# Kernel tuning notes

Measured on AMD Instinct MI355X. Metric: run time of the kernel, lower is better.

## Reference

```python
import jax, jax.numpy as jnp
import numpy as np

EMBED = 512
HEADS = 8
EPS = 1e-5


def setup_inputs() -> dict:
    key = jax.random.key(0)
    ks = jax.random.split(key, 8)
    B, Sq, Skv, D = 4, 2048, 2048, EMBED
    return {
        "layer_input": jax.random.normal(ks[0], (B, Sq, D), jnp.float32),
        "cross_attn_input": jax.random.normal(ks[1], (B, Skv, D), jnp.float32),
        "Wq": jax.random.normal(ks[2], (D, D), jnp.float32) * (D ** -0.5),
        "bq": jnp.zeros((D,), jnp.float32),
        "Wkv": jax.random.normal(ks[3], (D, 2 * D), jnp.float32) * (D ** -0.5),
        "bkv": jnp.zeros((2 * D,), jnp.float32),
        "Wo": jax.random.normal(ks[4], (D, D), jnp.float32) * (D ** -0.5),
        "bo": jnp.zeros((D,), jnp.float32),
        "gamma": jnp.ones((D,), jnp.float32),
        "beta": jnp.zeros((D,), jnp.float32),
    }


def _split_heads(x):
    # ... s (h d) -> ... h s d
    *lead, s, hd = x.shape
    d = hd // HEADS
    return jnp.moveaxis(x.reshape(*lead, s, HEADS, d), -2, -3)


def _merge_heads(x):
    # ... h s d -> ... s (h d)
    x = jnp.moveaxis(x, -3, -2)
    *lead, s, h, d = x.shape
    return x.reshape(*lead, s, h * d)


def reference(layer_input, cross_attn_input, Wq, bq, Wkv, bkv, Wo, bo, gamma, beta):
    scale = (EMBED // HEADS) ** -0.5
    res = layer_input
    q = layer_input @ Wq + bq
    kv = cross_attn_input @ Wkv + bkv
    k, v = jnp.split(kv, 2, axis=-1)
    q, k, v = map(_split_heads, (q, k, v))  # [B, H, S, d]
    scores = jnp.einsum('bhqc,bhkc->bhqk', q, k) * scale
    weights = jax.nn.softmax(scores, axis=-1)  # dropout p=0 -> identity
    out = jnp.einsum('bhqk,bhkc->bhqc', weights, v)
    out = _merge_heads(out)
    out = out @ Wo + bo
    x = out + res
    mu = jnp.mean(x, axis=-1, keepdims=True)
    var = jnp.mean(jnp.square(x - mu), axis=-1, keepdims=True)
    return (x - mu) * jax.lax.rsqrt(var + EPS) * gamma + beta
```

## Files before the change

kernel.cpp:

```cpp
#include <hip/hip_runtime.h>
#include <hip/hip_bf16.h>
#include <stdint.h>

#define SEQ    2048
#define DM     512
#define NHEAD  8
#define HD     64
#define BATCH  4
#define MTOT   (BATCH*SEQ)

typedef __attribute__((ext_vector_type(4))) float  f32x4;
typedef __attribute__((ext_vector_type(8))) short  bf16x8;
typedef __attribute__((ext_vector_type(8))) unsigned short u16x8;
typedef __attribute__((ext_vector_type(4))) unsigned short u16x4;
typedef __attribute__((ext_vector_type(4))) float  fl4;
typedef __attribute__((ext_vector_type(2))) unsigned u32x2;
typedef __attribute__((ext_vector_type(4))) unsigned u32x4;

__device__ __forceinline__ unsigned short f2bf(float f) {
  union { float f; unsigned u; } c; c.f = f;
  return (unsigned short)((c.u + 0x7fffu + ((c.u >> 16) & 1u)) >> 16);
}

__device__ __forceinline__ void load_lds16(const void* g, void* l) {
  __builtin_amdgcn_global_load_lds((__attribute__((address_space(1))) void*)g,
                                   (__attribute__((address_space(3))) void*)l,
                                   16, 0, 0);
}

__device__ __forceinline__ u32x2 ds_tr16(const void* p) {
  u32x2 r;
  asm volatile("ds_read_b64_tr_b16 %0, %1"
               : "=v"(r)
               : "v"((__attribute__((address_space(3))) const void*)p));
  return r;
}

__device__ __forceinline__ unsigned pack_bf2(float lo, float hi) {
  __hip_bfloat162 h2 = __float22bfloat162_rn(float2{lo, hi});
  unsigned u; __builtin_memcpy(&u, &h2, 4);
  return u;
}

__global__ void k_pre(const float* __restrict__ X, unsigned short* __restrict__ Xb,
                      const float* __restrict__ C, unsigned short* __restrict__ Cb,
                      const float* __restrict__ Wq, unsigned short* __restrict__ Wqt,
                      const float* __restrict__ Wkv, unsigned short* __restrict__ Wkvt,
                      const float* __restrict__ Wo, unsigned short* __restrict__ Wot) {
  __shared__ __align__(16) unsigned short t[64][66];
  int bid = blockIdx.x, tid = threadIdx.x;
  if (bid < 8192) {
    const float* src = (bid < 4096) ? X : C;
    unsigned short* dst = (bid < 4096) ? Xb : Cb;
    int i = (bid & 4095) * 256 + tid;
    fl4 v = *(const fl4*)(src + (size_t)i * 4);
    u32x2 o;
    o[0] = pack_bf2(v[0], v[1]);
    o[1] = pack_bf2(v[2], v[3]);
    *(u32x2*)((void*)(dst + (size_t)i * 4)) = o;
    return;
  }
  int tjob = bid - 8192;
  const float* W; unsigned short* Wt; int Nd, bx, by;
  if (tjob < 64)       { W = Wq;  Wt = Wqt;  Nd = 512;  bx = tjob & 7;  by = tjob >> 3; }
  else if (tjob < 192) { int u = tjob - 64;  W = Wkv; Wt = Wkvt; Nd = 1024; bx = u & 15; by = u >> 4; }
  else                 { int u = tjob - 192; W = Wo;  Wt = Wot;  Nd = 512;  bx = u & 7;  by = u >> 3; }
  int k0 = by * 64, n0 = bx * 64;
  int r = tid >> 2, cs = (tid & 3) * 16;
  const float* src = W + (size_t)(k0 + r) * Nd + n0 + cs;
#pragma unroll
  for (int i = 0; i < 4; ++i) {
    fl4 v = *(const fl4*)(src + i * 4);
    *(unsigned*)&t[r][cs + i*4]     = pack_bf2(v[0], v[1]);
    *(unsigned*)&t[r][cs + i*4 + 2] = pack_bf2(v[2], v[3]);
  }
  __syncthreads();
  unsigned short* drow = Wt + (size_t)(n0 + r) * 512 + k0 + cs;
#pragma unroll
  for (int half = 0; half < 2; ++half) {
    u16x8 o;
#pragma unroll
    for (int i = 0; i < 8; ++i) o[i] = t[cs + half*8 + i][r];
    *(u16x8*)(drow + half * 8) = o;
  }
}

template<int RESID>
__device__ __forceinline__ void gemm128x64(
    const unsigned short* __restrict__ A,
    const unsigned short* __restrict__ Bt,
    const float* __restrict__ bias,
    const float* __restrict__ res,
    void* __restrict__ Cout,
    int N, int K, int m0, int n0, float osc,
    unsigned short* Als, unsigned short* Bls) {
  int tid  = threadIdx.x;
  int lane = tid & 63, wave = tid >> 6;
  int q = lane & 15, lk = lane >> 4;
  f32x4 acc[2][4];
#pragma unroll
  for (int mt = 0; mt < 2; ++mt)
#pragma unroll
    for (int nt = 0; nt < 4; ++nt) acc[mt][nt] = f32x4{0.f,0.f,0.f,0.f};

  const unsigned short* gA[4];
#pragma unroll
  for (int it = 0; it < 4; ++it) {
    int idx = tid + it * 256;
    int row = idx >> 3, ch = idx & 7, sc = ch ^ (row & 7);
    gA[it] = A + (size_t)(m0 + row) * K + sc * 8;
  }
  const unsigned short* gB[2];
#pragma unroll
  for (int it = 0; it < 2; ++it) {
    int idx = tid + it * 256;
    int row = idx >> 3, ch = idx & 7, sc = ch ^ (row & 7);
    gB[it] = Bt + (size_t)(n0 + row) * K + sc * 8;
  }
  char* aD = (char*)Als + tid * 16;
  char* bD = (char*)Bls + tid * 16;

#pragma unroll
  for (int it = 0; it < 4; ++it) { load_lds16(gA[it], aD + it * 4096); gA[it] += 64; }
#pragma unroll
  for (int it = 0; it < 2; ++it) { load_lds16(gB[it], bD + it * 4096); gB[it] += 64; }
  __syncthreads();

  int nkb = K >> 6;
  int buf = 0;
  for (int kb = 0; kb < nkb; ++kb) {
    if (kb + 1 < nkb) {
      char* aN = aD + (buf ^ 1) * 16384;
      char* bN = bD + (buf ^ 1) * 8192;
#pragma unroll
      for (int it = 0; it < 4; ++it) { load_lds16(gA[it], aN + it * 4096); gA[it] += 64; }
#pragma unroll
      for (int it = 0; it < 2; ++it) { load_lds16(gB[it], bN + it * 4096); gB[it] += 64; }
    }
    const char* aR = (const char*)Als + buf * 16384;
    const char* bR = (const char*)Bls + buf * 8192;
#pragma unroll
    for (int ks = 0; ks < 2; ++ks) {
      bf16x8 a[2], b[4];
#pragma unroll
      for (int mt = 0; mt < 2; ++mt) {
        int row = wave * 32 + mt * 16 + q;
        a[mt] = *(const bf16x8*)(aR + row * 128 + (((ks*4 + lk) ^ (row & 7)) * 16));
      }
#pragma unroll
      for (int nt = 0; nt < 4; ++nt) {
        int row = nt * 16 + q;
        b[nt] = *(const bf16x8*)(bR + row * 128 + (((ks*4 + lk) ^ (row & 7)) * 16));
      }
#pragma unroll
      for (int mt = 0; mt < 2; ++mt)
#pragma unroll
        for (int nt = 0; nt < 4; ++nt)
          acc[mt][nt] = __builtin_amdgcn_mfma_f32_16x16x32_bf16(a[mt], b[nt], acc[mt][nt], 0, 0, 0);
    }
    __syncthreads();
    buf ^= 1;
  }
#pragma unroll
  for (int nt = 0; nt < 4; ++nt) {
    int col = n0 + nt * 16 + q;
    float bv = bias[col];
#pragma unroll
    for (int mt = 0; mt < 2; ++mt) {
      int rowb = m0 + wave * 32 + mt * 16 + lk * 4;
#pragma unroll
      for (int rr = 0; rr < 4; ++rr) {
        float v = acc[mt][nt][rr] + bv;
        size_t off = (size_t)(rowb + rr) * N + col;
        if (RESID) ((float*)Cout)[off] = v + res[off];
        else       ((unsigned short*)Cout)[off] = f2bf(v * osc);
      }
    }
  }
}

__global__ __launch_bounds__(256, 3)
void k_projmm(const unsigned short* __restrict__ Xb, const unsigned short* __restrict__ Cb,
              const unsigned short* __restrict__ Wqt, const unsigned short* __restrict__ Wkvt,
              const float* __restrict__ bq, const float* __restrict__ bkv,
              unsigned short* __restrict__ Qb, unsigned short* __restrict__ KVb) {
  __shared__ __align__(16) unsigned short Als[2 * 128 * 64];
  __shared__ __align__(16) unsigned short Bls[2 * 64 * 64];
  int bid = blockIdx.x;
  int l = (bid & 7) * 192 + (bid >> 3);
  const float c1 = 0.125f * 1.44269504088896340736f;
  if (l < 512) {
    int m = l >> 3, n = l & 7;
    gemm128x64<0>(Xb, Wqt, bq, nullptr, Qb, 512, 512, m * 128, n * 64, c1, Als, Bls);
  } else {
    int l2 = l - 512;
    int m = l2 >> 4, n = l2 & 15;
    gemm128x64<0>(Cb, Wkvt, bkv, nullptr, KVb, 1024, 512, m * 128, n * 64, 1.0f, Als, Bls);
  }
}

__global__ __launch_bounds__(256, 3)
void k_omm(const unsigned short* __restrict__ Abuf, const unsigned short* __restrict__ Wot,
           const float* __restrict__ bo, const float* __restrict__ resid,
           float* __restrict__ tmp) {
  __shared__ __align__(16) unsigned short Als[2 * 128 * 64];
  __shared__ __align__(16) unsigned short Bls[2 * 64 * 64];
  int bid = blockIdx.x;
  int l = (bid & 7) * 64 + (bid >> 3);
  int m = l >> 3, n = l & 7;
  gemm128x64<1>(Abuf, Wot, bo, resid, tmp, 512, 512, m * 128, n * 64, 1.0f, Als, Bls);
}

__global__ __launch_bounds__(256, 4)
void k_attn(const unsigned short* __restrict__ Qb,
            const unsigned short* __restrict__ KVb,
            unsigned short* __restrict__ Ab) {
  __shared__ __align__(16) unsigned short Klds[2][64 * 64];
  __shared__ __align__(16) unsigned short Vlds[3][4096];
  int tid  = threadIdx.x;
  int lane = tid & 63, wave = tid >> 6;
  int q    = lane & 15, lk = lane >> 4;
  int lkb0 = lk & 1, lkb1 = lk >> 1;
  int bid = blockIdx.x;
  int swz = (bid & 7) * 128 + (bid >> 3);
  int qt = swz & 31, bh = swz >> 5;
  int b  = bh >> 3, h = bh & 7;
  int q0 = qt * 64 + wave * 16;
  const size_t kvbase = (size_t)b * SEQ * 1024;

  bf16x8 qf0, qf1;
  {
    size_t qrow = (size_t)b * SEQ + q0 + q;
    qf0 = *(const bf16x8*)(Qb + qrow * DM + h * HD + lk * 8);
    qf1 = *(const bf16x8*)(Qb + qrow * DM + h * HD + 32 + lk * 8);
  }
  f32x4 acc[4];
#pragma unroll
  for (int i = 0; i < 4; ++i) acc[i] = f32x4{0.f,0.f,0.f,0.f};
  float l = 0.f;
  u32x4 pbA[2];

  const unsigned short *gK0, *gK1, *gV0, *gV1;
  {
    int r0 = tid >> 3, s0_ = (tid & 7) ^ (r0 & 7);
    gK0 = KVb + kvbase + (size_t)r0 * 1024 + h * HD + s0_ * 8;
    int i1 = tid + 256, r1 = i1 >> 3, s1_ = (i1 & 7) ^ (r1 & 7);
    gK1 = KVb + kvbase + (size_t)r1 * 1024 + h * HD + s1_ * 8;
    int dt0 = tid >> 7, w0 = tid & 127, p0 = w0 >> 1, c80 = (w0 & 1) * 8;
    int t0 = (p0 & 32) + (((p0 >> 2) & 3) << 3) + (((p0 >> 4) & 1) << 2) + (p0 & 3);
    gV0 = KVb + kvbase + (size_t)t0 * 1024 + 512 + h * HD + dt0 * 16 + c80;
    int i1v = tid + 256, dt1 = i1v >> 7, w1 = i1v & 127, p1 = w1 >> 1, c81 = (w1 & 1) * 8;
    int t1 = (p1 & 32) + (((p1 >> 2) & 3) << 3) + (((p1 >> 4) & 1) << 2) + (p1 & 3);
    gV1 = KVb + kvbase + (size_t)t1 * 1024 + 512 + h * HD + dt1 * 16 + c81;
  }
  char* kdA = (char*)Klds[0] + tid * 16;
  char* kdB = (char*)Klds[1] + tid * 16;
  char* vdA = (char*)Vlds[0] + tid * 16;
  char* vdB = (char*)Vlds[1] + tid * 16;
  char* vdC = (char*)Vlds[2] + tid * 16;
  const char* krA = (const char*)Klds[0];
  const char* krB = (const char*)Klds[1];
  const char* vsA = (const char*)Vlds[0] + lane * 8;
  const char* vsB = (const char*)Vlds[1] + lane * 8;
  const char* vsC = (const char*)Vlds[2] + lane * 8;

#define STAGE(kd_, vd_) do {                        \
    load_lds16(gK0, (kd_));                         \
    load_lds16(gK1, (kd_) + 4096);                  \
    load_lds16(gV0, (vd_));                         \
    load_lds16(gV1, (vd_) + 4096);                  \
    gK0 += 65536; gK1 += 65536;                     \
    gV0 += 65536; gV1 += 65536;                     \
  } while (0)

  STAGE(kdA, vdA);
  __syncthreads();

  const int NT = SEQ / 64;
  int kc = 0;
  int vn = 1;
  int vp = 2;
  for (int kb = 0; kb < NT; ++kb) {
    if (kb < NT - 1) {
      char* kd = kc ? kdA : kdB;
      char* vd = (vn == 0) ? vdA : ((vn == 1) ? vdB : vdC);
      STAGE(kd, vd);
    }

    u32x2 tr[4][2][2];
    if (kb > 0) {
      const char* vsrc = (vp == 0) ? vsA : ((vp == 1) ? vsB : vsC);
#pragma unroll
      for (int dt = 0; dt < 4; ++dt)
#pragma unroll
        for (int ks2 = 0; ks2 < 2; ++ks2)
#pragma unroll
          for (int u = 0; u < 2; ++u)
            tr[dt][ks2][u] = ds_tr16(vsrc + dt * 2048 + ks2 * 1024 + u * 512);
      asm volatile("s_waitcnt lgkmcnt(0)" ::: "memory");
      __builtin_amdgcn_sched_barrier(0);
      __builtin_amdgcn_s_setprio(1);
#pragma unroll
      for (int ks2 = 0; ks2 < 2; ++ks2) {
        union { u32x4 u; bf16x8 v; } pb;
        pb.u = pbA[ks2];
#pragma unroll
        for (int dt = 0; dt < 4; ++dt) {
          union { u32x4 u; bf16x8 v; } cv;
          cv.u[0] = tr[dt][ks2][0][0]; cv.u[1] = tr[dt][ks2][0][1];
          cv.u[2] = tr[dt][ks2][1][0]; cv.u[3] = tr[dt][ks2][1][1];
          acc[dt] = __builtin_amdgcn_mfma_f32_16x16x32_bf16(cv.v, pb.v, acc[dt], 0, 0, 0);
        }
      }
      __builtin_amdgcn_s_setprio(0);
    }

    const char* kr = kc ? krB : krA;
    f32x4 st[4];
#pragma unroll
    for (int kt = 0; kt < 4; ++kt) st[kt] = f32x4{0.f,0.f,0.f,0.f};
    __builtin_amdgcn_s_setprio(1);
#pragma unroll
    for (int kt = 0; kt < 4; ++kt) {
      int row = kt * 16 + q;
      bf16x8 kf0 = *(const bf16x8*)(kr + row * 128 + ((lk ^ (row & 7)) * 16));
      bf16x8 kf1 = *(const bf16x8*)(kr + row * 128 + (((4 + lk) ^ (row & 7)) * 16));
      st[kt] = __builtin_amdgcn_mfma_f32_16x16x32_bf16(kf0, qf0, st[kt], 0, 0, 0);
      st[kt] = __builtin_amdgcn_mfma_f32_16x16x32_bf16(kf1, qf1, st[kt], 0, 0, 0);
    }
    __builtin_amdgcn_s_setprio(0);

    float p[4][4];
#pragma unroll
    for (int kt = 0; kt < 4; ++kt)
#pragma unroll
      for (int r = 0; r < 4; ++r) {
        float pe = __builtin_amdgcn_exp2f(st[kt][r]);
        p[kt][r] = pe;
        l += pe;
      }
    unsigned pk[4][2];
#pragma unroll
    for (int kt = 0; kt < 4; ++kt)
#pragma unroll
      for (int rr = 0; rr < 2; ++rr)
        pk[kt][rr] = pack_bf2(p[kt][2*rr], p[kt][2*rr + 1]);
#pragma unroll
    for (int ks2 = 0; ks2 < 2; ++ks2)
#pragma unroll
      for (int rr = 0; rr < 2; ++rr) {
        unsigned a_ = pk[2*ks2][rr], b_ = pk[2*ks2 + 1][rr];
        unsigned E = lkb1 ? b_ : a_;
        unsigned O = lkb1 ? a_ : b_;
        unsigned A = __shfl_xor((int)E, 16);
        unsigned B = __shfl_xor((int)O, 32);
        unsigned C = __shfl_xor((int)O, 48);
        unsigned dlo = lkb1 ? (lkb0 ? A : B) : (lkb0 ? C : E);
        unsigned dhi = lkb1 ? (lkb0 ? E : C) : (lkb0 ? B : A);
        pbA[ks2][rr]     = dlo;
        pbA[ks2][2 + rr] = dhi;
      }

    __syncthreads();
    kc ^= 1;
    vn = (vn == 2) ? 0 : vn + 1;
    vp = (vp == 2) ? 0 : vp + 1;
  }

  {
    const char* vsrc = (vp == 0) ? vsA : ((vp == 1) ? vsB : vsC);
    u32x2 tr[4][2][2];
#pragma unroll
    for (int dt = 0; dt < 4; ++dt)
#pragma unroll
      for (int ks2 = 0; ks2 < 2; ++ks2)
#pragma unroll
        for (int u = 0; u < 2; ++u)
          tr[dt][ks2][u] = ds_tr16(vsrc + dt * 2048 + ks2 * 1024 + u * 512);
    asm volatile("s_waitcnt lgkmcnt(0)" ::: "memory");
    __builtin_amdgcn_sched_barrier(0);
#pragma unroll
    for (int ks2 = 0; ks2 < 2; ++ks2) {
      union { u32x4 u; bf16x8 v; } pb;
      pb.u = pbA[ks2];
#pragma unroll
      for (int dt = 0; dt < 4; ++dt) {
        union { u32x4 u; bf16x8 v; } cv;
        cv.u[0] = tr[dt][ks2][0][0]; cv.u[1] = tr[dt][ks2][0][1];
        cv.u[2] = tr[dt][ks2][1][0]; cv.u[3] = tr[dt][ks2][1][1];
        acc[dt] = __builtin_amdgcn_mfma_f32_16x16x32_bf16(cv.v, pb.v, acc[dt], 0, 0, 0);
      }
    }
  }

  l += __shfl_xor(l, 16);
  l += __shfl_xor(l, 32);

  float inv = 1.0f / l;
  size_t orow = ((size_t)b * SEQ + q0 + q) * DM + h * HD + lk * 4;
#pragma unroll
  for (int dt = 0; dt < 4; ++dt) {
    u16x4 o;
#pragma unroll
    for (int r = 0; r < 4; ++r) o[r] = f2bf(acc[dt][r] * inv);
    *(u16x4*)(Ab + orow + dt * 16) = o;
  }
#undef STAGE
}

__global__ void k_ln(const float* __restrict__ x, const float* __restrict__ gamma,
                     const float* __restrict__ beta, float* __restrict__ out) {
  int tid = threadIdx.x, lane = tid & 63, wave = tid >> 6;
  size_t row = (size_t)blockIdx.x * 4 + wave;
  const float* xr = x + row * DM + lane * 8;
  fl4 v0 = *(const fl4*)xr;
  fl4 v1 = *(const fl4*)(xr + 4);
  float s  = (v0[0]+v0[1]) + (v0[2]+v0[3]) + (v1[0]+v1[1]) + (v1[2]+v1[3]);
  float ss = (v0[0]*v0[0]+v0[1]*v0[1]) + (v0[2]*v0[2]+v0[3]*v0[3])
           + (v1[0]*v1[0]+v1[1]*v1[1]) + (v1[2]*v1[2]+v1[3]*v1[3]);
#pragma unroll
  for (int off = 1; off < 64; off <<= 1) {
    s  += __shfl_xor(s, off);
    ss += __shfl_xor(ss, off);
  }
  float mu  = s * (1.0f / DM);
  float var = ss * (1.0f / DM) - mu * mu;
  float w = rsqrtf(var + 1e-5f);
  fl4 g0 = *(const fl4*)(gamma + lane*8), g1 = *(const fl4*)(gamma + lane*8 + 4);
  fl4 b0 = *(const fl4*)(beta + lane*8),  b1 = *(const fl4*)(beta + lane*8 + 4);
  fl4 o0, o1;
#pragma unroll
  for (int i = 0; i < 4; ++i) {
    o0[i] = (v0[i] - mu) * w * g0[i] + b0[i];
    o1[i] = (v1[i] - mu) * w * g1[i] + b1[i];
  }
  float* orow = out + row * DM + lane * 8;
  *(fl4*)orow = o0;
  *(fl4*)(orow + 4) = o1;
}

extern "C" void kernel_launch(void* const* d_in, const int* in_sizes, int n_in,
                              void* d_out, int out_size, void* d_ws, size_t ws_size,
                              hipStream_t stream) {
  const float* layer_input = (const float*)d_in[0];
  const float* cross       = (const float*)d_in[1];
  const float* Wq   = (const float*)d_in[2];
  const float* bq   = (const float*)d_in[3];
  const float* Wkv  = (const float*)d_in[4];
  const float* bkv  = (const float*)d_in[5];
  const float* Wo   = (const float*)d_in[6];
  const float* bo   = (const float*)d_in[7];
  const float* gamma = (const float*)d_in[8];
  const float* beta  = (const float*)d_in[9];
  float* out = (float*)d_out;

  char* ws = (char*)d_ws;
  unsigned short* Xb   = (unsigned short*)(ws + (size_t)0);
  unsigned short* Cb   = (unsigned short*)(ws + ((size_t)8  << 20));
  unsigned short* Qb   = (unsigned short*)(ws + ((size_t)16 << 20));
  unsigned short* KVb  = (unsigned short*)(ws + ((size_t)24 << 20));
  unsigned short* Abuf = (unsigned short*)(ws + ((size_t)40 << 20));
  float*          tmp  = (float*)         (ws + ((size_t)48 << 20));
  unsigned short* Wqt  = (unsigned short*)(ws + ((size_t)64 << 20));
  unsigned short* Wkvt = (unsigned short*)(ws + ((size_t)65 << 20));
  unsigned short* Wot  = (unsigned short*)(ws + ((size_t)67 << 20));

  k_pre<<<8448, 256, 0, stream>>>(layer_input, Xb, cross, Cb,
                                  Wq, Wqt, Wkv, Wkvt, Wo, Wot);
  k_projmm<<<1536, 256, 0, stream>>>(Xb, Cb, Wqt, Wkvt, bq, bkv, Qb, KVb);
  k_attn<<<1024, 256, 0, stream>>>(Qb, KVb, Abuf);
  k_omm<<<512, 256, 0, stream>>>(Abuf, Wot, bo, layer_input, tmp);
  k_ln<<<MTOT/4, 256, 0, stream>>>(tmp, gamma, beta, out);
}
```

Measured before the change: 116.1 us.

## Process two 16-row query subtiles per wave in attention kernel

Each wave now handles 32 query rows (two 16-row halves) instead of 16, so every block covers a 128-query tile and the grid halves to 512 blocks. K and V fragments loaded from LDS are reused across both query halves, which halves the K/V global and LDS traffic per query row. The cost is roughly double the accumulator and score registers, so launch bounds drop to 2 blocks per CU. With only 512 blocks there is less parallelism to hide latency.

```diff
diff --git a/kernel.cpp b/kernel.cpp
--- a/kernel.cpp
+++ b/kernel.cpp
@@ -211,7 +211,7 @@
   gemm128x64<1>(Abuf, Wot, bo, resid, tmp, 512, 512, m * 128, n * 64, 1.0f, Als, Bls);
 }
 
-__global__ __launch_bounds__(256, 4)
+__global__ __launch_bounds__(256, 2)
 void k_attn(const unsigned short* __restrict__ Qb,
             const unsigned short* __restrict__ KVb,
             unsigned short* __restrict__ Ab) {
@@ -222,23 +222,26 @@
   int q    = lane & 15, lk = lane >> 4;
   int lkb0 = lk & 1, lkb1 = lk >> 1;
   int bid = blockIdx.x;
-  int swz = (bid & 7) * 128 + (bid >> 3);
-  int qt = swz & 31, bh = swz >> 5;
+  int swz = (bid & 7) * 64 + (bid >> 3);
+  int qt = swz & 15, bh = swz >> 4;
   int b  = bh >> 3, h = bh & 7;
-  int q0 = qt * 64 + wave * 16;
+  int q0 = qt * 128 + wave * 32;
   const size_t kvbase = (size_t)b * SEQ * 1024;
 
-  bf16x8 qf0, qf1;
-  {
-    size_t qrow = (size_t)b * SEQ + q0 + q;
-    qf0 = *(const bf16x8*)(Qb + qrow * DM + h * HD + lk * 8);
-    qf1 = *(const bf16x8*)(Qb + qrow * DM + h * HD + 32 + lk * 8);
-  }
-  f32x4 acc[4];
-#pragma unroll
-  for (int i = 0; i < 4; ++i) acc[i] = f32x4{0.f,0.f,0.f,0.f};
-  float l = 0.f;
-  u32x4 pbA[2];
+  bf16x8 qf[2][2];
+#pragma unroll
+  for (int qh = 0; qh < 2; ++qh) {
+    size_t qrow = (size_t)b * SEQ + q0 + qh * 16 + q;
+    qf[qh][0] = *(const bf16x8*)(Qb + qrow * DM + h * HD + lk * 8);
+    qf[qh][1] = *(const bf16x8*)(Qb + qrow * DM + h * HD + 32 + lk * 8);
+  }
+  f32x4 acc[2][4];
+#pragma unroll
+  for (int qh = 0; qh < 2; ++qh)
+#pragma unroll
+    for (int i = 0; i < 4; ++i) acc[qh][i] = f32x4{0.f,0.f,0.f,0.f};
+  float l[2] = {0.f, 0.f};
+  u32x4 pbA[2][2];
 
   const unsigned short *gK0, *gK1, *gV0, *gV1;
   {
@@ -287,9 +290,9 @@
       STAGE(kd, vd);
     }
 
-    u32x2 tr[4][2][2];
     if (kb > 0) {
       const char* vsrc = (vp == 0) ? vsA : ((vp == 1) ? vsB : vsC);
+      u32x2 tr[4][2][2];
 #pragma unroll
       for (int dt = 0; dt < 4; ++dt)
 #pragma unroll
@@ -302,64 +305,72 @@
       __builtin_amdgcn_s_setprio(1);
 #pragma unroll
       for (int ks2 = 0; ks2 < 2; ++ks2) {
-        union { u32x4 u; bf16x8 v; } pb;
-        pb.u = pbA[ks2];
+        union { u32x4 u; bf16x8 v; } pb0, pb1;
+        pb0.u = pbA[0][ks2]; pb1.u = pbA[1][ks2];
 #pragma unroll
         for (int dt = 0; dt < 4; ++dt) {
           union { u32x4 u; bf16x8 v; } cv;
           cv.u[0] = tr[dt][ks2][0][0]; cv.u[1] = tr[dt][ks2][0][1];
           cv.u[2] = tr[dt][ks2][1][0]; cv.u[3] = tr[dt][ks2][1][1];
-          acc[dt] = __builtin_amdgcn_mfma_f32_16x16x32_bf16(cv.v, pb.v, acc[dt], 0, 0, 0);
+          acc[0][dt] = __builtin_amdgcn_mfma_f32_16x16x32_bf16(cv.v, pb0.v, acc[0][dt], 0, 0, 0);
+          acc[1][dt] = __builtin_amdgcn_mfma_f32_16x16x32_bf16(cv.v, pb1.v, acc[1][dt], 0, 0, 0);
         }
       }
       __builtin_amdgcn_s_setprio(0);
     }
 
     const char* kr = kc ? krB : krA;
-    f32x4 st[4];
-#pragma unroll
-    for (int kt = 0; kt < 4; ++kt) st[kt] = f32x4{0.f,0.f,0.f,0.f};
+    f32x4 st[2][4];
+#pragma unroll
+    for (int qh = 0; qh < 2; ++qh)
+#pragma unroll
+      for (int kt = 0; kt < 4; ++kt) st[qh][kt] = f32x4{0.f,0.f,0.f,0.f};
     __builtin_amdgcn_s_setprio(1);
 #pragma unroll
     for (int kt = 0; kt < 4; ++kt) {
       int row = kt * 16 + q;
       bf16x8 kf0 = *(const bf16x8*)(kr + row * 128 + ((lk ^ (row & 7)) * 16));
       bf16x8 kf1 = *(const bf16x8*)(kr + row * 128 + (((4 + lk) ^ (row & 7)) * 16));
-      st[kt] = __builtin_amdgcn_mfma_f32_16x16x32_bf16(kf0, qf0, st[kt], 0, 0, 0);
-      st[kt] = __builtin_amdgcn_mfma_f32_16x16x32_bf16(kf1, qf1, st[kt], 0, 0, 0);
+      st[0][kt] = __builtin_amdgcn_mfma_f32_16x16x32_bf16(kf0, qf[0][0], st[0][kt], 0, 0, 0);
+      st[0][kt] = __builtin_amdgcn_mfma_f32_16x16x32_bf16(kf1, qf[0][1], st[0][kt], 0, 0, 0);
+      st[1][kt] = __builtin_amdgcn_mfma_f32_16x16x32_bf16(kf0, qf[1][0], st[1][kt], 0, 0, 0);
+      st[1][kt] = __builtin_amdgcn_mfma_f32_16x16x32_bf16(kf1, qf[1][1], st[1][kt], 0, 0, 0);
     }
     __builtin_amdgcn_s_setprio(0);
 
-    float p[4][4];
-#pragma unroll
-    for (int kt = 0; kt < 4; ++kt)
-#pragma unroll
-      for (int r = 0; r < 4; ++r) {
-        float pe = __builtin_amdgcn_exp2f(st[kt][r]);
-        p[kt][r] = pe;
-        l += pe;
-      }
-    unsigned pk[4][2];
-#pragma unroll
-    for (int kt = 0; kt < 4; ++kt)
-#pragma unroll
-      for (int rr = 0; rr < 2; ++rr)
-        pk[kt][rr] = pack_bf2(p[kt][2*rr], p[kt][2*rr + 1]);
-#pragma unroll
-    for (int ks2 = 0; ks2 < 2; ++ks2)
-#pragma unroll
-      for (int rr = 0; rr < 2; ++rr) {
-        unsigned a_ = pk[2*ks2][rr], b_ = pk[2*ks2 + 1][rr];
-        unsigned E = lkb1 ? b_ : a_;
-        unsigned O = lkb1 ? a_ : b_;
-        unsigned A = __shfl_xor((int)E, 16);
-        unsigned B = __shfl_xor((int)O, 32);
-        unsigned C = __shfl_xor((int)O, 48);
-        unsigned dlo = lkb1 ? (lkb0 ? A : B) : (lkb0 ? C : E);
-        unsigned dhi = lkb1 ? (lkb0 ? E : C) : (lkb0 ? B : A);
-        pbA[ks2][rr]     = dlo;
-        pbA[ks2][2 + rr] = dhi;
-      }
+#pragma unroll
+    for (int qh = 0; qh < 2; ++qh) {
+      float p[4][4];
+#pragma unroll
+      for (int kt = 0; kt < 4; ++kt)
+#pragma unroll
+        for (int r = 0; r < 4; ++r) {
+          float pe = __builtin_amdgcn_exp2f(st[qh][kt][r]);
+          p[kt][r] = pe;
+          l[qh] += pe;
+        }
+      unsigned pk[4][2];
+#pragma unroll
+      for (int kt = 0; kt < 4; ++kt)
+#pragma unroll
+        for (int rr = 0; rr < 2; ++rr)
+          pk[kt][rr] = pack_bf2(p[kt][2*rr], p[kt][2*rr + 1]);
+#pragma unroll
+      for (int ks2 = 0; ks2 < 2; ++ks2)
+#pragma unroll
+        for (int rr = 0; rr < 2; ++rr) {
+          unsigned a_ = pk[2*ks2][rr], b_ = pk[2*ks2 + 1][rr];
+          unsigned E = lkb1 ? b_ : a_;
+          unsigned O = lkb1 ? a_ : b_;
+          unsigned A = __shfl_xor((int)E, 16);
+          unsigned B = __shfl_xor((int)O, 32);
+          unsigned C = __shfl_xor((int)O, 48);
+          unsigned dlo = lkb1 ? (lkb0 ? A : B) : (lkb0 ? C : E);
+          unsigned dhi = lkb1 ? (lkb0 ? E : C) : (lkb0 ? B : A);
+          pbA[qh][ks2][rr]     = dlo;
+          pbA[qh][ks2][2 + rr] = dhi;
+        }
+    }
 
     __syncthreads();
     kc ^= 1;
@@ -381,29 +392,33 @@
     __builtin_amdgcn_sched_barrier(0);
 #pragma unroll
     for (int ks2 = 0; ks2 < 2; ++ks2) {
-      union { u32x4 u; bf16x8 v; } pb;
-      pb.u = pbA[ks2];
+      union { u32x4 u; bf16x8 v; } pb0, pb1;
+      pb0.u = pbA[0][ks2]; pb1.u = pbA[1][ks2];
 #pragma unroll
       for (int dt = 0; dt < 4; ++dt) {
         union { u32x4 u; bf16x8 v; } cv;
         cv.u[0] = tr[dt][ks2][0][0]; cv.u[1] = tr[dt][ks2][0][1];
         cv.u[2] = tr[dt][ks2][1][0]; cv.u[3] = tr[dt][ks2][1][1];
-        acc[dt] = __builtin_amdgcn_mfma_f32_16x16x32_bf16(cv.v, pb.v, acc[dt], 0, 0, 0);
+        acc[0][dt] = __builtin_amdgcn_mfma_f32_16x16x32_bf16(cv.v, pb0.v, acc[0][dt], 0, 0, 0);
+        acc[1][dt] = __builtin_amdgcn_mfma_f32_16x16x32_bf16(cv.v, pb1.v, acc[1][dt], 0, 0, 0);
       }
     }
   }
 
-  l += __shfl_xor(l, 16);
-  l += __shfl_xor(l, 32);
-
-  float inv = 1.0f / l;
-  size_t orow = ((size_t)b * SEQ + q0 + q) * DM + h * HD + lk * 4;
-#pragma unroll
-  for (int dt = 0; dt < 4; ++dt) {
-    u16x4 o;
-#pragma unroll
-    for (int r = 0; r < 4; ++r) o[r] = f2bf(acc[dt][r] * inv);
-    *(u16x4*)(Ab + orow + dt * 16) = o;
+#pragma unroll
+  for (int qh = 0; qh < 2; ++qh) {
+    float lv = l[qh];
+    lv += __shfl_xor(lv, 16);
+    lv += __shfl_xor(lv, 32);
+    float inv = 1.0f / lv;
+    size_t orow = ((size_t)b * SEQ + q0 + qh * 16 + q) * DM + h * HD + lk * 4;
+#pragma unroll
+    for (int dt = 0; dt < 4; ++dt) {
+      u16x4 o;
+#pragma unroll
+      for (int r = 0; r < 4; ++r) o[r] = f2bf(acc[qh][dt][r] * inv);
+      *(u16x4*)(Ab + orow + dt * 16) = o;
+    }
   }
 #undef STAGE
 }
@@ -468,7 +483,7 @@
   k_pre<<<8448, 256, 0, stream>>>(layer_input, Xb, cross, Cb,
                                   Wq, Wqt, Wkv, Wkvt, Wo, Wot);
   k_projmm<<<1536, 256, 0, stream>>>(Xb, Cb, Wqt, Wkvt, bq, bkv, Qb, KVb);
-  k_attn<<<1024, 256, 0, stream>>>(Qb, KVb, Abuf);
+  k_attn<<<512, 256, 0, stream>>>(Qb, KVb, Abuf);
   k_omm<<<512, 256, 0, stream>>>(Abuf, Wot, bo, layer_input, tmp);
   k_ln<<<MTOT/4, 256, 0, stream>>>(tmp, gamma, beta, out);
 }
```

New measurement: 115.2 us. Within noise of the previous version (-0.8%).

## Load K directly into registers in attention; use bf16 residual and pre-LN buffer

Applied to the files above, without the earlier changes.

The attention kernel drops the K shared-memory double buffer. Each lane now loads its K fragments straight from global memory into registers, prefetching the next tile right after the QK MFMAs, so K staging and LDS reads go away and LDS use falls. Separately, the output projection now reads the bf16 copy of the layer input as the residual and writes the pre-LayerNorm sum as bf16, which halves traffic in k_omm and k_ln. The cost is extra rounding in the residual path, and each wave does uncoalesced, redundant global K loads that are no longer shared across waves through LDS.

```diff
diff --git a/kernel.cpp b/kernel.cpp
--- a/kernel.cpp
+++ b/kernel.cpp
@@ -20,6 +20,12 @@
 __device__ __forceinline__ unsigned short f2bf(float f) {
   union { float f; unsigned u; } c; c.f = f;
   return (unsigned short)((c.u + 0x7fffu + ((c.u >> 16) & 1u)) >> 16);
+}
+
+__device__ __forceinline__ float bf2f(unsigned short s) {
+  unsigned u = (unsigned)s << 16;
+  float f; __builtin_memcpy(&f, &u, 4);
+  return f;
 }
 
 __device__ __forceinline__ void load_lds16(const void* g, void* l) {
@@ -90,8 +96,8 @@
     const unsigned short* __restrict__ A,
     const unsigned short* __restrict__ Bt,
     const float* __restrict__ bias,
-    const float* __restrict__ res,
-    void* __restrict__ Cout,
+    const unsigned short* __restrict__ res,
+    unsigned short* __restrict__ Cout,
     int N, int K, int m0, int n0, float osc,
     unsigned short* Als, unsigned short* Bls) {
   int tid  = threadIdx.x;
@@ -172,8 +178,8 @@
       for (int rr = 0; rr < 4; ++rr) {
         float v = acc[mt][nt][rr] + bv;
         size_t off = (size_t)(rowb + rr) * N + col;
-        if (RESID) ((float*)Cout)[off] = v + res[off];
-        else       ((unsigned short*)Cout)[off] = f2bf(v * osc);
+        if (RESID) Cout[off] = f2bf(v + bf2f(res[off]));
+        else       Cout[off] = f2bf(v * osc);
       }
     }
   }
@@ -201,21 +207,20 @@
 
 __global__ __launch_bounds__(256, 3)
 void k_omm(const unsigned short* __restrict__ Abuf, const unsigned short* __restrict__ Wot,
-           const float* __restrict__ bo, const float* __restrict__ resid,
-           float* __restrict__ tmp) {
+           const float* __restrict__ bo, const unsigned short* __restrict__ residb,
+           unsigned short* __restrict__ tmp) {
   __shared__ __align__(16) unsigned short Als[2 * 128 * 64];
   __shared__ __align__(16) unsigned short Bls[2 * 64 * 64];
   int bid = blockIdx.x;
   int l = (bid & 7) * 64 + (bid >> 3);
   int m = l >> 3, n = l & 7;
-  gemm128x64<1>(Abuf, Wot, bo, resid, tmp, 512, 512, m * 128, n * 64, 1.0f, Als, Bls);
+  gemm128x64<1>(Abuf, Wot, bo, residb, tmp, 512, 512, m * 128, n * 64, 1.0f, Als, Bls);
 }
 
 __global__ __launch_bounds__(256, 4)
 void k_attn(const unsigned short* __restrict__ Qb,
             const unsigned short* __restrict__ KVb,
             unsigned short* __restrict__ Ab) {
-  __shared__ __align__(16) unsigned short Klds[2][64 * 64];
   __shared__ __align__(16) unsigned short Vlds[3][4096];
   int tid  = threadIdx.x;
   int lane = tid & 63, wave = tid >> 6;
@@ -240,12 +245,13 @@
   float l = 0.f;
   u32x4 pbA[2];
 
-  const unsigned short *gK0, *gK1, *gV0, *gV1;
+  const unsigned short* gK[4];
+#pragma unroll
+  for (int kt = 0; kt < 4; ++kt)
+    gK[kt] = KVb + kvbase + (size_t)(kt * 16 + q) * 1024 + h * HD + lk * 8;
+
+  const unsigned short *gV0, *gV1;
   {
-    int r0 = tid >> 3, s0_ = (tid & 7) ^ (r0 & 7);
-    gK0 = KVb + kvbase + (size_t)r0 * 1024 + h * HD + s0_ * 8;
-    int i1 = tid + 256, r1 = i1 >> 3, s1_ = (i1 & 7) ^ (r1 & 7);
-    gK1 = KVb + kvbase + (size_t)r1 * 1024 + h * HD + s1_ * 8;
     int dt0 = tid >> 7, w0 = tid & 127, p0 = w0 >> 1, c80 = (w0 & 1) * 8;
     int t0 = (p0 & 32) + (((p0 >> 2) & 3) << 3) + (((p0 >> 4) & 1) << 2) + (p0 & 3);
     gV0 = KVb + kvbase + (size_t)t0 * 1024 + 512 + h * HD + dt0 * 16 + c80;
@@ -253,43 +259,41 @@
     int t1 = (p1 & 32) + (((p1 >> 2) & 3) << 3) + (((p1 >> 4) & 1) << 2) + (p1 & 3);
     gV1 = KVb + kvbase + (size_t)t1 * 1024 + 512 + h * HD + dt1 * 16 + c81;
   }
-  char* kdA = (char*)Klds[0] + tid * 16;
-  char* kdB = (char*)Klds[1] + tid * 16;
   char* vdA = (char*)Vlds[0] + tid * 16;
   char* vdB = (char*)Vlds[1] + tid * 16;
   char* vdC = (char*)Vlds[2] + tid * 16;
-  const char* krA = (const char*)Klds[0];
-  const char* krB = (const char*)Klds[1];
   const char* vsA = (const char*)Vlds[0] + lane * 8;
   const char* vsB = (const char*)Vlds[1] + lane * 8;
   const char* vsC = (const char*)Vlds[2] + lane * 8;
 
-#define STAGE(kd_, vd_) do {                        \
-    load_lds16(gK0, (kd_));                         \
-    load_lds16(gK1, (kd_) + 4096);                  \
+#define STAGE_V(vd_) do {                           \
     load_lds16(gV0, (vd_));                         \
     load_lds16(gV1, (vd_) + 4096);                  \
-    gK0 += 65536; gK1 += 65536;                     \
     gV0 += 65536; gV1 += 65536;                     \
   } while (0)
 
-  STAGE(kdA, vdA);
+  bf16x8 kreg[4][2];
+#pragma unroll
+  for (int kt = 0; kt < 4; ++kt) {
+    kreg[kt][0] = *(const bf16x8*)gK[kt];
+    kreg[kt][1] = *(const bf16x8*)(gK[kt] + 32);
+    gK[kt] += 65536;
+  }
+  STAGE_V(vdA);
   __syncthreads();
 
   const int NT = SEQ / 64;
-  int kc = 0;
   int vn = 1;
   int vp = 2;
   for (int kb = 0; kb < NT; ++kb) {
     if (kb < NT - 1) {
-      char* kd = kc ? kdA : kdB;
       char* vd = (vn == 0) ? vdA : ((vn == 1) ? vdB : vdC);
-      STAGE(kd, vd);
-    }
-
-    u32x2 tr[4][2][2];
+      STAGE_V(vd);
+    }
+
     if (kb > 0) {
       const char* vsrc = (vp == 0) ? vsA : ((vp == 1) ? vsB : vsC);
+      u32x2 tr[4][2][2];
 #pragma unroll
       for (int dt = 0; dt < 4; ++dt)
 #pragma unroll
@@ -315,20 +319,25 @@
       __builtin_amdgcn_s_setprio(0);
     }
 
-    const char* kr = kc ? krB : krA;
     f32x4 st[4];
 #pragma unroll
     for (int kt = 0; kt < 4; ++kt) st[kt] = f32x4{0.f,0.f,0.f,0.f};
     __builtin_amdgcn_s_setprio(1);
 #pragma unroll
     for (int kt = 0; kt < 4; ++kt) {
-      int row = kt * 16 + q;
-      bf16x8 kf0 = *(const bf16x8*)(kr + row * 128 + ((lk ^ (row & 7)) * 16));
-      bf16x8 kf1 = *(const bf16x8*)(kr + row * 128 + (((4 + lk) ^ (row & 7)) * 16));
-      st[kt] = __builtin_amdgcn_mfma_f32_16x16x32_bf16(kf0, qf0, st[kt], 0, 0, 0);
-      st[kt] = __builtin_amdgcn_mfma_f32_16x16x32_bf16(kf1, qf1, st[kt], 0, 0, 0);
+      st[kt] = __builtin_amdgcn_mfma_f32_16x16x32_bf16(kreg[kt][0], qf0, st[kt], 0, 0, 0);
+      st[kt] = __builtin_amdgcn_mfma_f32_16x16x32_bf16(kreg[kt][1], qf1, st[kt], 0, 0, 0);
     }
     __builtin_amdgcn_s_setprio(0);
+
+    if (kb < NT - 1) {
+#pragma unroll
+      for (int kt = 0; kt < 4; ++kt) {
+        kreg[kt][0] = *(const bf16x8*)gK[kt];
+        kreg[kt][1] = *(const bf16x8*)(gK[kt] + 32);
+        gK[kt] += 65536;
+      }
+    }
 
     float p[4][4];
 #pragma unroll
@@ -362,7 +371,6 @@
       }
 
     __syncthreads();
-    kc ^= 1;
     vn = (vn == 2) ? 0 : vn + 1;
     vp = (vp == 2) ? 0 : vp + 1;
   }
@@ -395,7 +403,6 @@
 
   l += __shfl_xor(l, 16);
   l += __shfl_xor(l, 32);
-
   float inv = 1.0f / l;
   size_t orow = ((size_t)b * SEQ + q0 + q) * DM + h * HD + lk * 4;
 #pragma unroll
@@ -405,19 +412,20 @@
     for (int r = 0; r < 4; ++r) o[r] = f2bf(acc[dt][r] * inv);
     *(u16x4*)(Ab + orow + dt * 16) = o;
   }
-#undef STAGE
-}
-
-__global__ void k_ln(const float* __restrict__ x, const float* __restrict__ gamma,
+#undef STAGE_V
+}
+
+__global__ void k_ln(const unsigned short* __restrict__ x, const float* __restrict__ gamma,
                      const float* __restrict__ beta, float* __restrict__ out) {
   int tid = threadIdx.x, lane = tid & 63, wave = tid >> 6;
   size_t row = (size_t)blockIdx.x * 4 + wave;
-  const float* xr = x + row * DM + lane * 8;
-  fl4 v0 = *(const fl4*)xr;
-  fl4 v1 = *(const fl4*)(xr + 4);
-  float s  = (v0[0]+v0[1]) + (v0[2]+v0[3]) + (v1[0]+v1[1]) + (v1[2]+v1[3]);
-  float ss = (v0[0]*v0[0]+v0[1]*v0[1]) + (v0[2]*v0[2]+v0[3]*v0[3])
-           + (v1[0]*v1[0]+v1[1]*v1[1]) + (v1[2]*v1[2]+v1[3]*v1[3]);
+  u16x8 xv = *(const u16x8*)(x + row * DM + lane * 8);
+  float v[8];
+#pragma unroll
+  for (int i = 0; i < 8; ++i) v[i] = bf2f(xv[i]);
+  float s  = (v[0]+v[1]) + (v[2]+v[3]) + (v[4]+v[5]) + (v[6]+v[7]);
+  float ss = (v[0]*v[0]+v[1]*v[1]) + (v[2]*v[2]+v[3]*v[3])
+           + (v[4]*v[4]+v[5]*v[5]) + (v[6]*v[6]+v[7]*v[7]);
 #pragma unroll
   for (int off = 1; off < 64; off <<= 1) {
     s  += __shfl_xor(s, off);
@@ -431,8 +439,8 @@
   fl4 o0, o1;
 #pragma unroll
   for (int i = 0; i < 4; ++i) {
-    o0[i] = (v0[i] - mu) * w * g0[i] + b0[i];
-    o1[i] = (v1[i] - mu) * w * g1[i] + b1[i];
+    o0[i] = (v[i]     - mu) * w * g0[i] + b0[i];
+    o1[i] = (v[4 + i] - mu) * w * g1[i] + b1[i];
   }
   float* orow = out + row * DM + lane * 8;
   *(fl4*)orow = o0;
@@ -460,7 +468,7 @@
   unsigned short* Qb   = (unsigned short*)(ws + ((size_t)16 << 20));
   unsigned short* KVb  = (unsigned short*)(ws + ((size_t)24 << 20));
   unsigned short* Abuf = (unsigned short*)(ws + ((size_t)40 << 20));
-  float*          tmp  = (float*)         (ws + ((size_t)48 << 20));
+  unsigned short* tmpb = (unsigned short*)(ws + ((size_t)48 << 20));
   unsigned short* Wqt  = (unsigned short*)(ws + ((size_t)64 << 20));
   unsigned short* Wkvt = (unsigned short*)(ws + ((size_t)65 << 20));
   unsigned short* Wot  = (unsigned short*)(ws + ((size_t)67 << 20));
@@ -469,6 +477,6 @@
                                   Wq, Wqt, Wkv, Wkvt, Wo, Wot);
   k_projmm<<<1536, 256, 0, stream>>>(Xb, Cb, Wqt, Wkvt, bq, bkv, Qb, KVb);
   k_attn<<<1024, 256, 0, stream>>>(Qb, KVb, Abuf);
-  k_omm<<<512, 256, 0, stream>>>(Abuf, Wot, bo, layer_input, tmp);
-  k_ln<<<MTOT/4, 256, 0, stream>>>(tmp, gamma, beta, out);
-}
+  k_omm<<<512, 256, 0, stream>>>(Abuf, Wot, bo, Xb, tmpb);
+  k_ln<<<MTOT/4, 256, 0, stream>>>(tmpb, gamma, beta, out);
+}
```

After: 187.2 us. 1.61x slower.
